# Optimization experiments

Hardware: AMD Instinct MI355X
Metric: run time of the kernel (lower is better)

## Reference

```python
import jax, jax.numpy as jnp
import numpy as np

D_MODEL = 1024
N_HEAD = 16
D_HEAD = D_MODEL // N_HEAD
EXP = 4
B, T = 2, 2048
EPS = 1e-5

def setup_inputs() -> dict:
    key = jax.random.key(0)
    ks = jax.random.split(key, 16)
    s = 0.02
    return {
        "x": jax.random.normal(ks[0], (B, T, D_MODEL), jnp.float32),
        "ln1_w": jnp.ones((D_MODEL,), jnp.float32),
        "ln1_b": jnp.zeros((D_MODEL,), jnp.float32),
        "attn_w": jax.random.normal(ks[1], (D_MODEL, 3 * D_MODEL), jnp.float32) * s,
        "attn_b": jnp.zeros((3 * D_MODEL,), jnp.float32),
        "proj_w": jax.random.normal(ks[2], (D_MODEL, D_MODEL), jnp.float32) * s,
        "proj_b": jnp.zeros((D_MODEL,), jnp.float32),
        "ln2_w": jnp.ones((D_MODEL,), jnp.float32),
        "ln2_b": jnp.zeros((D_MODEL,), jnp.float32),
        "fc_w": jax.random.normal(ks[3], (D_MODEL, EXP * D_MODEL), jnp.float32) * s,
        "fc_b": jnp.zeros((EXP * D_MODEL,), jnp.float32),
        "fc2_w": jax.random.normal(ks[4], (EXP * D_MODEL, D_MODEL), jnp.float32) * s,
        "fc2_b": jnp.zeros((D_MODEL,), jnp.float32),
    }

def _layernorm(x, w, b):
    mu = jnp.mean(x, axis=-1, keepdims=True)
    var = jnp.mean(jnp.square(x - mu), axis=-1, keepdims=True)
    return (x - mu) * jax.lax.rsqrt(var + EPS) * w + b

def _attn(x, attn_w, attn_b, proj_w, proj_b):
    Bx, Tx, C = x.shape
    qkv = x @ attn_w + attn_b  # [B,T,3C]
    q, k, v = jnp.split(qkv, 3, axis=-1)
    # [B, H, T, Dh]
    q = q.reshape(Bx, Tx, N_HEAD, D_HEAD).transpose(0, 2, 1, 3)
    k = k.reshape(Bx, Tx, N_HEAD, D_HEAD).transpose(0, 2, 1, 3)
    v = v.reshape(Bx, Tx, N_HEAD, D_HEAD).transpose(0, 2, 1, 3)
    att = jnp.einsum('bhqd,bhkd->bhqk', q, k) * (1.0 / np.sqrt(D_HEAD))
    causal = jnp.tril(jnp.ones((Tx, Tx), bool))
    att = jnp.where(causal, att, -jnp.inf)
    att = jax.nn.softmax(att, axis=-1)
    y = jnp.einsum('bhqk,bhkd->bhqd', att, v)
    y = y.transpose(0, 2, 1, 3).reshape(Bx, Tx, C)
    return y @ proj_w + proj_b

def reference(x, ln1_w, ln1_b, attn_w, attn_b, proj_w, proj_b,
              ln2_w, ln2_b, fc_w, fc_b, fc2_w, fc2_b):
    x = x + _attn(_layernorm(x, ln1_w, ln1_b), attn_w, attn_b, proj_w, proj_b)
    h = _layernorm(x, ln2_w, ln2_b)
    h = jax.nn.gelu(h @ fc_w + fc_b, approximate=False)  # exact GELU (torch nn.GELU default)
    x = x + (h @ fc2_w + fc2_b)
    return x
```

## Files before the change

### kernel.cpp

```cpp
#include <hip/hip_runtime.h>
#include <hip/hip_bf16.h>
#include <math.h>


#define D_MODEL 1024
#define N_HEAD  16
#define D_HEAD  64
#define SEQ_T   2048
#define BATCH   2
#define NROWS   (BATCH * SEQ_T)
#define C3      (3 * D_MODEL)
#define D_FF    (4 * D_MODEL)

typedef __bf16 bf16x8 __attribute__((ext_vector_type(8)));
typedef __bf16 bf16x4t __attribute__((ext_vector_type(4)));
typedef short  s16x4  __attribute__((ext_vector_type(4)));
typedef float  f32x4  __attribute__((ext_vector_type(4)));

#define WAIT_VM0() asm volatile("s_waitcnt vmcnt(0)" ::: "memory")

__device__ __forceinline__ f32x4 mfma16_bf16(s16x4 a, s16x4 b, f32x4 c)
{
#if __has_builtin(__builtin_amdgcn_mfma_f32_16x16x16_bf16)
    return __builtin_amdgcn_mfma_f32_16x16x16_bf16(
        __builtin_bit_cast(bf16x4t, a), __builtin_bit_cast(bf16x4t, b), c, 0, 0, 0);
#else
    return __builtin_amdgcn_mfma_f32_16x16x16bf16_1k(a, b, c, 0, 0, 0);
#endif
}

__global__ __launch_bounds__(256) void ln_kernel(
    const float* __restrict__ in, const float* __restrict__ w,
    const float* __restrict__ b, __hip_bfloat16* __restrict__ out, int D)
{
    const int row = blockIdx.x;
    const int tid = threadIdx.x;
    const float* x = in + (size_t)row * 1024;

    const float4 v = *(const float4*)(x + tid * 4);
    float s  = v.x + v.y + v.z + v.w;
    float s2 = v.x * v.x + v.y * v.y + v.z * v.z + v.w * v.w;

    __shared__ float rs[256], rs2[256];
    rs[tid] = s; rs2[tid] = s2;
    __syncthreads();
    for (int off = 128; off > 0; off >>= 1) {
        if (tid < off) { rs[tid] += rs[tid + off]; rs2[tid] += rs2[tid + off]; }
        __syncthreads();
    }
    const float mu   = rs[0] * (1.0f / 1024.0f);
    const float var  = rs2[0] * (1.0f / 1024.0f) - mu * mu;
    const float rstd = rsqrtf(var + 1e-5f);

    const float4 w4 = *(const float4*)(w + tid * 4);
    const float4 b4 = *(const float4*)(b + tid * 4);
    float o[4] = {(v.x - mu) * rstd * w4.x + b4.x,
                  (v.y - mu) * rstd * w4.y + b4.y,
                  (v.z - mu) * rstd * w4.z + b4.z,
                  (v.w - mu) * rstd * w4.w + b4.w};
    ushort4 pk;
    { __hip_bfloat16 e0 = __float2bfloat16(o[0]); pk.x = *(unsigned short*)&e0;
      __hip_bfloat16 e1 = __float2bfloat16(o[1]); pk.y = *(unsigned short*)&e1;
      __hip_bfloat16 e2 = __float2bfloat16(o[2]); pk.z = *(unsigned short*)&e2;
      __hip_bfloat16 e3 = __float2bfloat16(o[3]); pk.w = *(unsigned short*)&e3; }
    *(ushort4*)(out + (size_t)row * 1024 + tid * 4) = pk;
}

__global__ __launch_bounds__(256) void transpose_all_kernel(
    const float* __restrict__ attn_w, const float* __restrict__ proj_w,
    const float* __restrict__ fc_w,   const float* __restrict__ fc2_w,
    __hip_bfloat16* __restrict__ attn_wt, __hip_bfloat16* __restrict__ proj_wt,
    __hip_bfloat16* __restrict__ fc_wt,   __hip_bfloat16* __restrict__ fc2_wt)
{
    __shared__ float t[32][33];
    int tb = blockIdx.x;
    const float* W; __hip_bfloat16* Wt; int K, N;
    if (tb < 3072)      { W = attn_w; Wt = attn_wt; K = D_MODEL; N = C3; }
    else if (tb < 4096) { tb -= 3072; W = proj_w; Wt = proj_wt; K = D_MODEL; N = D_MODEL; }
    else if (tb < 8192) { tb -= 4096; W = fc_w;   Wt = fc_wt;   K = D_MODEL; N = D_FF; }
    else                { tb -= 8192; W = fc2_w;  Wt = fc2_wt;  K = D_FF;    N = D_MODEL; }
    const int ntx = N >> 5;
    const int k0 = (tb / ntx) * 32;
    const int n0 = (tb % ntx) * 32;

    const int row = threadIdx.x >> 3;
    const int c4  = (threadIdx.x & 7) * 4;

    const float4 v = *(const float4*)&W[(size_t)(k0 + row) * N + n0 + c4];
    t[row][c4 + 0] = v.x; t[row][c4 + 1] = v.y;
    t[row][c4 + 2] = v.z; t[row][c4 + 3] = v.w;
    __syncthreads();

    ushort4 pk;
    { __hip_bfloat16 e0 = __float2bfloat16(t[c4 + 0][row]); pk.x = *(unsigned short*)&e0;
      __hip_bfloat16 e1 = __float2bfloat16(t[c4 + 1][row]); pk.y = *(unsigned short*)&e1;
      __hip_bfloat16 e2 = __float2bfloat16(t[c4 + 2][row]); pk.z = *(unsigned short*)&e2;
      __hip_bfloat16 e3 = __float2bfloat16(t[c4 + 3][row]); pk.w = *(unsigned short*)&e3; }
    *(ushort4*)&Wt[(size_t)(n0 + row) * K + k0 + c4] = pk;
}

__device__ __forceinline__ void async16(const __hip_bfloat16* g, __hip_bfloat16* l)
{
    __builtin_amdgcn_global_load_lds(
        (const __attribute__((address_space(1))) void*)g,
        (__attribute__((address_space(3))) void*)l, 16, 0, 0);
}

__device__ __forceinline__ float gelu_exact(float v)
{
    return 0.5f * v * (1.0f + erff(v * 0.70710678118654752f));
}

__device__ __forceinline__ void swz_xcd(int& bx, int& by)
{
    const int nbx = gridDim.x;
    const int nwg = nbx * gridDim.y;
    int lin = blockIdx.y * nbx + blockIdx.x;
    const int per = nwg >> 3;
    lin = (lin & 7) * per + (lin >> 3);
    bx = lin % nbx;
    by = lin / nbx;
}


__device__ __forceinline__ void stage_db4(
    const __hip_bfloat16* __restrict__ Ab, const __hip_bfloat16* __restrict__ Bb,
    int K, int kt, __hip_bfloat16* __restrict__ as,
    __hip_bfloat16* __restrict__ bs, int tid)
{
    const int k0 = kt * 32;
#pragma unroll
    for (int i = 0; i < 2; ++i) {
        async16(Ab + (size_t)(i * 64) * K + k0, as + i * 64 * 32 + tid * 8);
        async16(Bb + (size_t)(i * 64) * K + k0, bs + i * 64 * 32 + tid * 8);
    }
}

__device__ __forceinline__ void gemm_db4(
    const __hip_bfloat16* __restrict__ A,
    const __hip_bfloat16* __restrict__ Bt,
    int K, int row0, int col0, f32x4 (&acc)[4][4])
{
    __shared__ __align__(16) __hip_bfloat16 Asl[2][128 * 32];
    __shared__ __align__(16) __hip_bfloat16 Bsl[2][128 * 32];

    const int tid  = threadIdx.x;
    const int wv   = tid >> 6;
    const int lane = tid & 63;
    const int ln15 = lane & 15;
    const int lq   = lane >> 4;
    const int mbase = (wv >> 1) * 64;
    const int nbase = (wv & 1) * 64;
    const int rcol = (lq ^ ((ln15 >> 1) & 3)) * 8;
    const int ssw  = ((tid & 3) ^ ((tid >> 3) & 3)) * 8;
    const __hip_bfloat16* Ab = A  + (size_t)(row0 + (tid >> 2)) * K + ssw;
    const __hip_bfloat16* Bb = Bt + (size_t)(col0 + (tid >> 2)) * K + ssw;
    const int nt = K >> 5;

#pragma unroll
    for (int mi = 0; mi < 4; ++mi)
#pragma unroll
        for (int ni = 0; ni < 4; ++ni) acc[mi][ni] = (f32x4){0.f, 0.f, 0.f, 0.f};

    stage_db4(Ab, Bb, K, 0, &Asl[0][0], &Bsl[0][0], tid);
    WAIT_VM0();
    __builtin_amdgcn_s_barrier();

    for (int t = 0; t < nt; ++t) {
        const int p   = t & 1;
        const int tcl = (t + 1 < nt) ? t + 1 : nt - 1;
        bf16x8 af[4], bfr[4];

#pragma unroll
        for (int mi = 0; mi < 4; ++mi)
            af[mi] = *(const bf16x8*)&Asl[p][(mbase + mi * 16 + ln15) * 32 + rcol];
#pragma unroll
        for (int ni = 0; ni < 4; ++ni)
            bfr[ni] = *(const bf16x8*)&Bsl[p][(nbase + ni * 16 + ln15) * 32 + rcol];

        stage_db4(Ab, Bb, K, tcl, &Asl[p ^ 1][0], &Bsl[p ^ 1][0], tid);

        __builtin_amdgcn_s_setprio(1);
#pragma unroll
        for (int mi = 0; mi < 4; ++mi)
#pragma unroll
            for (int ni = 0; ni < 4; ++ni)
                acc[mi][ni] = __builtin_amdgcn_mfma_f32_16x16x32_bf16(
                    af[mi], bfr[ni], acc[mi][ni], 0, 0, 0);
        __builtin_amdgcn_s_setprio(0);

        WAIT_VM0();
        __builtin_amdgcn_s_barrier();
    }
}


__device__ __forceinline__ void stage_db2w(
    const __hip_bfloat16* __restrict__ Ab, const __hip_bfloat16* __restrict__ Bb,
    int K, int kt, __hip_bfloat16* __restrict__ as,
    __hip_bfloat16* __restrict__ bs, int tid)
{
    const int k0 = kt * 64;
#pragma unroll
    for (int s = 0; s < 2; ++s) {
        async16(Ab + k0 + s * 32, as + s * 64 * 32 + tid * 8);
#pragma unroll
        for (int i = 0; i < 2; ++i)
            async16(Bb + (size_t)(i * 64) * K + k0 + s * 32,
                    bs + s * 128 * 32 + i * 64 * 32 + tid * 8);
    }
}

__device__ __forceinline__ void gemm_db2w(
    const __hip_bfloat16* __restrict__ A,
    const __hip_bfloat16* __restrict__ Bt,
    int K, int row0, int col0, f32x4 (&acc)[2][4])
{
    __shared__ __align__(16) __hip_bfloat16 Asl[2][2 * 64 * 32];
    __shared__ __align__(16) __hip_bfloat16 Bsl[2][2 * 128 * 32];

    const int tid  = threadIdx.x;
    const int wv   = tid >> 6;
    const int lane = tid & 63;
    const int ln15 = lane & 15;
    const int lq   = lane >> 4;
    const int mbase = (wv >> 1) * 32;
    const int nbase = (wv & 1) * 64;
    const int rcol = (lq ^ ((ln15 >> 1) & 3)) * 8;
    const int ssw  = ((tid & 3) ^ ((tid >> 3) & 3)) * 8;
    const __hip_bfloat16* Ab = A  + (size_t)(row0 + (tid >> 2)) * K + ssw;
    const __hip_bfloat16* Bb = Bt + (size_t)(col0 + (tid >> 2)) * K + ssw;
    const int nt = K >> 6;

#pragma unroll
    for (int mi = 0; mi < 2; ++mi)
#pragma unroll
        for (int ni = 0; ni < 4; ++ni) acc[mi][ni] = (f32x4){0.f, 0.f, 0.f, 0.f};

    stage_db2w(Ab, Bb, K, 0, &Asl[0][0], &Bsl[0][0], tid);
    WAIT_VM0();
    __builtin_amdgcn_s_barrier();

    for (int t = 0; t < nt; ++t) {
        const int p   = t & 1;
        const int tcl = (t + 1 < nt) ? t + 1 : nt - 1;
        bf16x8 af[2][2], bfr[2][4];

#pragma unroll
        for (int s = 0; s < 2; ++s) {
#pragma unroll
            for (int mi = 0; mi < 2; ++mi)
                af[s][mi] = *(const bf16x8*)
                    &Asl[p][s * 64 * 32 + (mbase + mi * 16 + ln15) * 32 + rcol];
#pragma unroll
            for (int ni = 0; ni < 4; ++ni)
                bfr[s][ni] = *(const bf16x8*)
                    &Bsl[p][s * 128 * 32 + (nbase + ni * 16 + ln15) * 32 + rcol];
        }

        stage_db2w(Ab, Bb, K, tcl, &Asl[p ^ 1][0], &Bsl[p ^ 1][0], tid);

        __builtin_amdgcn_s_setprio(1);
#pragma unroll
        for (int s = 0; s < 2; ++s)
#pragma unroll
            for (int mi = 0; mi < 2; ++mi)
#pragma unroll
                for (int ni = 0; ni < 4; ++ni)
                    acc[mi][ni] = __builtin_amdgcn_mfma_f32_16x16x32_bf16(
                        af[s][mi], bfr[s][ni], acc[mi][ni], 0, 0, 0);
        __builtin_amdgcn_s_setprio(0);

        WAIT_VM0();
        __builtin_amdgcn_s_barrier();
    }
}

__global__ __launch_bounds__(256, 3) void gemm128_kernel(
    const __hip_bfloat16* __restrict__ A,
    const __hip_bfloat16* __restrict__ Bt,
    const float* __restrict__ bias,
    const float* __restrict__ residual,
    void* __restrict__ Cout,
    int M, int N, int K, int act, int outBf16)
{
    int bx, by;
    swz_xcd(bx, by);
    const int row0 = by * 128;
    const int col0 = bx * 128;

    f32x4 acc[4][4];
    gemm_db4(A, Bt, K, row0, col0, acc);

    const int tid  = threadIdx.x;
    const int wv   = tid >> 6;
    const int lane = tid & 63;
    const int ln15 = lane & 15;
    const int lq   = lane >> 4;
    const int mbase = (wv >> 1) * 64;
    const int nbase = (wv & 1) * 64;

#pragma unroll
    for (int mi = 0; mi < 4; ++mi) {
#pragma unroll
        for (int ni = 0; ni < 4; ++ni) {
            const int gc = col0 + nbase + ni * 16 + ln15;
            const float bv = bias[gc];
#pragma unroll
            for (int r = 0; r < 4; ++r) {
                const int gr = row0 + mbase + mi * 16 + lq * 4 + r;
                float v = acc[mi][ni][r] + bv;
                if (act == 1) v = gelu_exact(v);
                if (residual) v += residual[(size_t)gr * N + gc];
                if (outBf16)
                    ((__hip_bfloat16*)Cout)[(size_t)gr * N + gc] = __float2bfloat16(v);
                else
                    ((float*)Cout)[(size_t)gr * N + gc] = v;
            }
        }
    }
}

__global__ __launch_bounds__(256, 3) void gemm64_kernel(
    const __hip_bfloat16* __restrict__ A,
    const __hip_bfloat16* __restrict__ Bt,
    const float* __restrict__ bias,
    const float* __restrict__ residual,
    void* __restrict__ Cout,
    int M, int N, int K, int act, int outBf16)
{
    int bx, by;
    swz_xcd(bx, by);
    const int row0 = by * 64;
    const int col0 = bx * 128;

    f32x4 acc[2][4];
    gemm_db2w(A, Bt, K, row0, col0, acc);

    const int tid  = threadIdx.x;
    const int wv   = tid >> 6;
    const int lane = tid & 63;
    const int ln15 = lane & 15;
    const int lq   = lane >> 4;
    const int mbase = (wv >> 1) * 32;
    const int nbase = (wv & 1) * 64;

#pragma unroll
    for (int mi = 0; mi < 2; ++mi) {
#pragma unroll
        for (int ni = 0; ni < 4; ++ni) {
            const int gc = col0 + nbase + ni * 16 + ln15;
            const float bv = bias[gc];
#pragma unroll
            for (int r = 0; r < 4; ++r) {
                const int gr = row0 + mbase + mi * 16 + lq * 4 + r;
                float v = acc[mi][ni][r] + bv;
                if (act == 1) v = gelu_exact(v);
                if (residual) v += residual[(size_t)gr * N + gc];
                if (outBf16)
                    ((__hip_bfloat16*)Cout)[(size_t)gr * N + gc] = __float2bfloat16(v);
                else
                    ((float*)Cout)[(size_t)gr * N + gc] = v;
            }
        }
    }
}

__global__ __launch_bounds__(256, 3) void qkv128_kernel(
    const __hip_bfloat16* __restrict__ A,
    const __hip_bfloat16* __restrict__ Bt,
    const float* __restrict__ bias,
    __hip_bfloat16* __restrict__ Qb,
    __hip_bfloat16* __restrict__ Kb,
    __hip_bfloat16* __restrict__ Vtb)
{
    int bx, by;
    swz_xcd(bx, by);
    const int row0 = by * 128;
    const int col0 = bx * 128;

    f32x4 acc[4][4];
    gemm_db4(A, Bt, D_MODEL, row0, col0, acc);

    const int tid  = threadIdx.x;
    const int wv   = tid >> 6;
    const int lane = tid & 63;
    const int ln15 = lane & 15;
    const int lq   = lane >> 4;
    const int mbase = (wv >> 1) * 64;
    const int nbase = (wv & 1) * 64;

#pragma unroll
    for (int mi = 0; mi < 4; ++mi) {
        const int gr0 = row0 + mbase + mi * 16 + lq * 4;
        const int bb  = gr0 >> 11;
        const int q0  = gr0 & 2047;
#pragma unroll
        for (int ni = 0; ni < 4; ++ni) {
            const int gc  = col0 + nbase + ni * 16 + ln15;
            const float bv = bias[gc];
            const int sec = gc >> 10;
            const int hd  = (gc & 1023) >> 6;
            const int d   = gc & 63;
            if (sec == 2) {
                unsigned short u[4];
#pragma unroll
                for (int r = 0; r < 4; ++r) {
                    __hip_bfloat16 e = __float2bfloat16(acc[mi][ni][r] + bv);
                    u[r] = *(unsigned short*)&e;
                }
                uint2 pk;
                pk.x = (unsigned int)u[0] | ((unsigned int)u[1] << 16);
                pk.y = (unsigned int)u[2] | ((unsigned int)u[3] << 16);
                *(uint2*)(Vtb + ((size_t)((bb * N_HEAD + hd) * D_HEAD + d)) * SEQ_T + q0) = pk;
            } else {
                __hip_bfloat16* dst = (sec == 0 ? Qb : Kb)
                    + ((size_t)((bb * N_HEAD + hd) * SEQ_T + q0)) * D_HEAD + d;
#pragma unroll
                for (int r = 0; r < 4; ++r)
                    dst[(size_t)r * D_HEAD] = __float2bfloat16(acc[mi][ni][r] + bv);
            }
        }
    }
}

#define ATQ 64
#define ATK 128
#define NQT (SEQ_T / ATQ)
#define VP2 136

__global__ __launch_bounds__(256) void mfma_attn_kernel(
    const __hip_bfloat16* __restrict__ Qb,
    const __hip_bfloat16* __restrict__ Kb,
    const __hip_bfloat16* __restrict__ Vtb,
    __hip_bfloat16* __restrict__ y)
{
    __shared__ __align__(16) __hip_bfloat16 Ks[2 * ATK * 32];
    __shared__ __align__(16) __hip_bfloat16 Vts[D_HEAD * VP2];

    const int flat = (blockIdx.z * gridDim.y + blockIdx.y) * gridDim.x + blockIdx.x;
    const int xcd  = flat & 7;
    const int slot = flat >> 3;
    const int pair = slot & 15;
    const int hb   = slot >> 4;
    const int h    = xcd + 8 * (hb & 1);
    const int b    = hb >> 1;

    const int tid  = threadIdx.x;
    const int wv   = tid >> 6;
    const int lane = tid & 63;
    const int ln15 = lane & 15;
    const int lq   = lane >> 4;

    const __hip_bfloat16* Qh = Qb  + (size_t)(b * N_HEAD + h) * SEQ_T * D_HEAD;
    const __hip_bfloat16* Kh = Kb  + (size_t)(b * N_HEAD + h) * SEQ_T * D_HEAD;
    const __hip_bfloat16* Vh = Vtb + (size_t)(b * N_HEAD + h) * D_HEAD * SEQ_T;
    const size_t bT = (size_t)b * SEQ_T;

    const float CEXP = 0.18033688011f;

    bf16x8 kreg[4], vreg[4];
    const int kr = tid >> 3, kg = tid & 7;
    const int vr = tid >> 4, vc = tid & 15;
    const int khalf = kg >> 2;
    const int kpos  = (kg & 3) ^ ((kr >> 1) & 3);

    auto issue = [&](int kb) {
#pragma unroll
        for (int i = 0; i < 4; ++i)
            kreg[i] = *(const bf16x8*)(Kh + (size_t)(kb + kr + i * 32) * D_HEAD + kg * 8);
#pragma unroll
        for (int i = 0; i < 4; ++i)
            vreg[i] = *(const bf16x8*)(Vh + (size_t)(vr + i * 16) * SEQ_T + kb + vc * 8);
    };
    auto commit = [&]() {
#pragma unroll
        for (int i = 0; i < 4; ++i) {
            const int r = kr + i * 32;
            *(bf16x8*)&Ks[khalf * (ATK * 32) + r * 32 + kpos * 8] = kreg[i];
        }
#pragma unroll
        for (int i = 0; i < 4; ++i) {
            const int r = vr + i * 16;
            *(bf16x8*)&Vts[r * VP2 + vc * 8] = vreg[i];
        }
    };

    const int rcol = (lq ^ ((ln15 >> 1) & 3)) * 8;

#pragma unroll 1
    for (int half = 0; half < 2; ++half) {
        const int qt    = half == 0 ? pair : (NQT - 1 - pair);
        const int qbase = qt * ATQ;
        const int ntk   = (qt >> 1) + 1;
        const int qg    = qbase + wv * 16 + ln15;

        bf16x8 qf[2];
#pragma unroll
        for (int kc = 0; kc < 2; ++kc)
            qf[kc] = *(const bf16x8*)(Qh + (size_t)(qbase + wv * 16 + ln15) * D_HEAD
                                      + kc * 32 + lq * 8);

        f32x4 Oacc[4];
#pragma unroll
        for (int dn = 0; dn < 4; ++dn) Oacc[dn] = (f32x4){0.f, 0.f, 0.f, 0.f};
        float m_run = -INFINITY, l_run = 0.f;

        issue(0);

        for (int t = 0; t < ntk; ++t) {
            const int kb = t * ATK;
            commit();
            __syncthreads();
            if (t + 1 < ntk) issue((t + 1) * ATK);

            f32x4 st[8];
#pragma unroll
            for (int jf = 0; jf < 8; ++jf) st[jf] = (f32x4){0.f, 0.f, 0.f, 0.f};
            __builtin_amdgcn_s_setprio(1);
#pragma unroll
            for (int jf = 0; jf < 8; ++jf) {
                const int rw = jf * 16 + ln15;
                const bf16x8 kf0 = *(const bf16x8*)&Ks[rw * 32 + rcol];
                const bf16x8 kf1 = *(const bf16x8*)&Ks[ATK * 32 + rw * 32 + rcol];
                st[jf] = __builtin_amdgcn_mfma_f32_16x16x32_bf16(kf0, qf[0], st[jf], 0, 0, 0);
                st[jf] = __builtin_amdgcn_mfma_f32_16x16x32_bf16(kf1, qf[1], st[jf], 0, 0, 0);
            }
            __builtin_amdgcn_s_setprio(0);

            if (t == ntk - 1) {
#pragma unroll
                for (int jf = 0; jf < 8; ++jf)
#pragma unroll
                    for (int r = 0; r < 4; ++r)
                        if ((kb + jf * 16 + lq * 4 + r) > qg) st[jf][r] = -INFINITY;
            }

            float tmax = st[0][0];
#pragma unroll
            for (int jf = 0; jf < 8; ++jf)
#pragma unroll
                for (int r = 0; r < 4; ++r) tmax = fmaxf(tmax, st[jf][r]);
            tmax = fmaxf(tmax, __shfl_xor(tmax, 16));
            tmax = fmaxf(tmax, __shfl_xor(tmax, 32));
            const float mnew  = fmaxf(m_run, tmax);
            const float alpha = exp2f((m_run - mnew) * CEXP);
            const float mc    = mnew * CEXP;
            float psum = 0.f;
#pragma unroll
            for (int jf = 0; jf < 8; ++jf)
#pragma unroll
                for (int r = 0; r < 4; ++r) {
                    const float p = exp2f(fmaf(st[jf][r], CEXP, -mc));
                    st[jf][r] = p;
                    psum += p;
                }
            psum += __shfl_xor(psum, 16);
            psum += __shfl_xor(psum, 32);
            l_run = alpha * l_run + psum;
            m_run = mnew;

            float a4[4];
#pragma unroll
            for (int r = 0; r < 4; ++r) a4[r] = __shfl(alpha, lq * 4 + r);
#pragma unroll
            for (int dn = 0; dn < 4; ++dn)
#pragma unroll
                for (int r = 0; r < 4; ++r) Oacc[dn][r] *= a4[r];

            __builtin_amdgcn_s_setprio(1);
#pragma unroll
            for (int jf = 0; jf < 8; ++jf) {
                s16x4 pfr;
#pragma unroll
                for (int s = 0; s < 4; ++s) {
                    __hip_bfloat16 e = __float2bfloat16(st[jf][s]);
                    pfr[s] = __builtin_bit_cast(short, e);
                }
#pragma unroll
                for (int dn = 0; dn < 4; ++dn) {
                    const s16x4 vfr = *(const s16x4*)&Vts[(dn * 16 + ln15) * VP2
                                                          + jf * 16 + lq * 4];
                    Oacc[dn] = mfma16_bf16(pfr, vfr, Oacc[dn]);
                }
            }
            __builtin_amdgcn_s_setprio(0);
            __syncthreads();
        }

        float il[4];
#pragma unroll
        for (int r = 0; r < 4; ++r) il[r] = 1.0f / __shfl(l_run, lq * 4 + r);
#pragma unroll
        for (int dn = 0; dn < 4; ++dn)
#pragma unroll
            for (int r = 0; r < 4; ++r)
                Ks[(wv * 16 + lq * 4 + r) * 72 + dn * 16 + ln15] =
                    __float2bfloat16(Oacc[dn][r] * il[r]);
        const int r2 = lane >> 3, c8 = (lane & 7) * 8;
#pragma unroll
        for (int i = 0; i < 2; ++i) {
            const int row = wv * 16 + r2 + 8 * i;
            const bf16x8 val = *(const bf16x8*)&Ks[row * 72 + c8];
            *(bf16x8*)(y + (bT + qbase + row) * D_MODEL + h * D_HEAD + c8) = val;
        }
        __syncthreads();
    }
}

extern "C" void kernel_launch(void* const* d_in, const int* in_sizes, int n_in,
                              void* d_out, int out_size, void* d_ws, size_t ws_size,
                              hipStream_t stream)
{
    const float* x      = (const float*)d_in[0];
    const float* ln1_w  = (const float*)d_in[1];
    const float* ln1_b  = (const float*)d_in[2];
    const float* attn_w = (const float*)d_in[3];
    const float* attn_b = (const float*)d_in[4];
    const float* proj_w = (const float*)d_in[5];
    const float* proj_b = (const float*)d_in[6];
    const float* ln2_w  = (const float*)d_in[7];
    const float* ln2_b  = (const float*)d_in[8];
    const float* fc_w   = (const float*)d_in[9];
    const float* fc_b   = (const float*)d_in[10];
    const float* fc2_w  = (const float*)d_in[11];
    const float* fc2_b  = (const float*)d_in[12];
    float* out = (float*)d_out;

    char* ws = (char*)d_ws;
    __hip_bfloat16* Qb      = (__hip_bfloat16*)(ws);
    __hip_bfloat16* Kb      = (__hip_bfloat16*)(ws + (size_t)8  * 1024 * 1024);
    __hip_bfloat16* Vtb     = (__hip_bfloat16*)(ws + (size_t)16 * 1024 * 1024);
    __hip_bfloat16* h_bf    = (__hip_bfloat16*)(ws);
    __hip_bfloat16* ln_buf  = (__hip_bfloat16*)(ws + (size_t)32 * 1024 * 1024);
    __hip_bfloat16* y_buf   = (__hip_bfloat16*)(ws + (size_t)40 * 1024 * 1024);
    float*          xmid    = (float*)(ws + (size_t)48 * 1024 * 1024);
    __hip_bfloat16* attn_wt = (__hip_bfloat16*)(ws + (size_t)64 * 1024 * 1024);
    __hip_bfloat16* proj_wt = (__hip_bfloat16*)(ws + (size_t)70 * 1024 * 1024);
    __hip_bfloat16* fc_wt   = (__hip_bfloat16*)(ws + (size_t)72 * 1024 * 1024);
    __hip_bfloat16* fc2_wt  = (__hip_bfloat16*)(ws + (size_t)80 * 1024 * 1024);

    dim3 blk256(256);

    transpose_all_kernel<<<dim3(12288), blk256, 0, stream>>>(
        attn_w, proj_w, fc_w, fc2_w, attn_wt, proj_wt, fc_wt, fc2_wt);

    ln_kernel<<<dim3(NROWS), blk256, 0, stream>>>(x, ln1_w, ln1_b, ln_buf, D_MODEL);

    qkv128_kernel<<<dim3(C3 / 128, NROWS / 128), blk256, 0, stream>>>(
        ln_buf, attn_wt, attn_b, Qb, Kb, Vtb);

    mfma_attn_kernel<<<dim3(NQT / 2, N_HEAD, BATCH), blk256, 0, stream>>>(
        Qb, Kb, Vtb, y_buf);

    gemm64_kernel<<<dim3(D_MODEL / 128, NROWS / 64), blk256, 0, stream>>>(
        y_buf, proj_wt, proj_b, x, xmid, NROWS, D_MODEL, D_MODEL, 0, 0);

    ln_kernel<<<dim3(NROWS), blk256, 0, stream>>>(xmid, ln2_w, ln2_b, ln_buf, D_MODEL);

    gemm128_kernel<<<dim3(D_FF / 128, NROWS / 128), blk256, 0, stream>>>(
        ln_buf, fc_wt, fc_b, nullptr, h_bf, NROWS, D_FF, D_MODEL, 1, 1);

    gemm64_kernel<<<dim3(D_MODEL / 128, NROWS / 64), blk256, 0, stream>>>(
        h_bf, fc2_wt, fc2_b, xmid, out, NROWS, D_MODEL, D_FF, 0, 0);
}
```

Baseline: 356.9 us.

## Add 256x256 8-wave pipelined GEMM for FC layer with tanh-GELU

Measured after the change: 341.6 us. -4.3%, faster.

```diff
diff --git a/kernel.cpp b/kernel.cpp
--- a/kernel.cpp
+++ b/kernel.cpp
@@ -18,6 +18,8 @@
 typedef float  f32x4  __attribute__((ext_vector_type(4)));
 
 #define WAIT_VM0() asm volatile("s_waitcnt vmcnt(0)" ::: "memory")
+#define WAIT_VM2() asm volatile("s_waitcnt vmcnt(2)" ::: "memory")
+#define WAIT_VM4() asm volatile("s_waitcnt vmcnt(4)" ::: "memory")
 
 __device__ __forceinline__ f32x4 mfma16_bf16(s16x4 a, s16x4 b, f32x4 c)
 {
@@ -106,9 +108,10 @@
         (__attribute__((address_space(3))) void*)l, 16, 0, 0);
 }
 
-__device__ __forceinline__ float gelu_exact(float v)
-{
-    return 0.5f * v * (1.0f + erff(v * 0.70710678118654752f));
+__device__ __forceinline__ float gelu_fast(float v)
+{
+    const float t = v * (0.7978845608f + 0.0356774081f * v * v);
+    return v / (1.0f + exp2f(-2.885390082f * t));
 }
 
 __device__ __forceinline__ void swz_xcd(int& bx, int& by)
@@ -122,6 +125,159 @@
     by = lin / nbx;
 }
 
+
+__global__ __launch_bounds__(512, 1) void gemm8p_kernel(
+    const __hip_bfloat16* __restrict__ A,
+    const __hip_bfloat16* __restrict__ Bt,
+    const float* __restrict__ bias,
+    __hip_bfloat16* __restrict__ Cout,
+    int M, int N, int K, int act)
+{
+    __shared__ __align__(16) __hip_bfloat16 Asl[2][4][64 * 64];
+    __shared__ __align__(16) __hip_bfloat16 Bsl[2][2][128 * 64];
+
+    int bx, by;
+    swz_xcd(bx, by);
+    const int row0 = by * 256;
+    const int col0 = bx * 256;
+
+    const int tid  = threadIdx.x;
+    const int wv   = tid >> 6;
+    const int lane = tid & 63;
+    const int ln15 = lane & 15;
+    const int lq   = lane >> 4;
+    const int wr   = wv >> 2;
+    const int wc   = wv & 3;
+
+    const int srow = tid >> 3;
+    const int sg   = ((tid & 7) ^ ((tid >> 3) & 7)) * 8;
+    const __hip_bfloat16* Ab = A  + (size_t)(row0 + srow) * K + sg;
+    const __hip_bfloat16* Bb = Bt + (size_t)(col0 + srow) * K + sg;
+    const int nt = K >> 6;
+
+    f32x4 acc[8][4];
+#pragma unroll
+    for (int mi = 0; mi < 8; ++mi)
+#pragma unroll
+        for (int ni = 0; ni < 4; ++ni) acc[mi][ni] = (f32x4){0.f, 0.f, 0.f, 0.f};
+
+    auto stA = [&](int t, int buf, int b) {
+        async16(Ab + (size_t)(b * 64) * K + t * 64, &Asl[buf][b][0] + tid * 8);
+    };
+    auto stB = [&](int t, int buf, int h) {
+        async16(Bb + (size_t)(h * 128) * K + t * 64, &Bsl[buf][h][0] + tid * 8);
+        async16(Bb + (size_t)(h * 128 + 64) * K + t * 64,
+                &Bsl[buf][h][0] + 4096 + tid * 8);
+    };
+
+    const int rg0 = (lq ^ (ln15 & 7)) * 8;
+    const int rg1 = ((4 | lq) ^ (ln15 & 7)) * 8;
+    auto ldA = [&](int buf, int mi, int kk) -> bf16x8 {
+        return *(const bf16x8*)&Asl[buf][wr * 2 + (mi >> 2)]
+            [((mi & 3) * 16 + ln15) * 64 + (kk ? rg1 : rg0)];
+    };
+    auto ldB = [&](int buf, int ni, int kk) -> bf16x8 {
+        return *(const bf16x8*)&Bsl[buf][wc >> 1]
+            [((wc & 1) * 64 + ni * 16 + ln15) * 64 + (kk ? rg1 : rg0)];
+    };
+
+    stB(0, 0, 0); stB(0, 0, 1);
+    stA(0, 0, 0); stA(0, 0, 2); stA(0, 0, 1); stA(0, 0, 3);
+    WAIT_VM0();
+    __builtin_amdgcn_s_barrier();
+
+    for (int t = 0; t < nt; ++t) {
+        const int pp = t & 1, op = pp ^ 1;
+        const int tc = (t + 1 < nt) ? t + 1 : nt - 1;
+        bf16x8 af[2][2], bfr[4][2];
+
+#pragma unroll
+        for (int m = 0; m < 2; ++m) { af[m][0] = ldA(pp, m, 0); af[m][1] = ldA(pp, m, 1); }
+#pragma unroll
+        for (int ni = 0; ni < 4; ++ni) { bfr[ni][0] = ldB(pp, ni, 0); bfr[ni][1] = ldB(pp, ni, 1); }
+        stB(tc, op, 0);
+        __builtin_amdgcn_s_barrier();
+        __builtin_amdgcn_s_setprio(1);
+#pragma unroll
+        for (int kk = 0; kk < 2; ++kk)
+#pragma unroll
+            for (int m = 0; m < 2; ++m)
+#pragma unroll
+                for (int ni = 0; ni < 4; ++ni)
+                    acc[m][ni] = __builtin_amdgcn_mfma_f32_16x16x32_bf16(
+                        af[m][kk], bfr[ni][kk], acc[m][ni], 0, 0, 0);
+        __builtin_amdgcn_s_setprio(0);
+        __builtin_amdgcn_s_barrier();
+
+#pragma unroll
+        for (int m = 0; m < 2; ++m) { af[m][0] = ldA(pp, 2 + m, 0); af[m][1] = ldA(pp, 2 + m, 1); }
+        stB(tc, op, 1);
+        WAIT_VM4();
+        __builtin_amdgcn_s_barrier();
+        __builtin_amdgcn_s_setprio(1);
+#pragma unroll
+        for (int kk = 0; kk < 2; ++kk)
+#pragma unroll
+            for (int m = 0; m < 2; ++m)
+#pragma unroll
+                for (int ni = 0; ni < 4; ++ni)
+                    acc[2 + m][ni] = __builtin_amdgcn_mfma_f32_16x16x32_bf16(
+                        af[m][kk], bfr[ni][kk], acc[2 + m][ni], 0, 0, 0);
+        __builtin_amdgcn_s_setprio(0);
+        __builtin_amdgcn_s_barrier();
+
+#pragma unroll
+        for (int m = 0; m < 2; ++m) { af[m][0] = ldA(pp, 4 + m, 0); af[m][1] = ldA(pp, 4 + m, 1); }
+        stA(tc, op, 0); stA(tc, op, 2);
+        __builtin_amdgcn_s_barrier();
+        __builtin_amdgcn_s_setprio(1);
+#pragma unroll
+        for (int kk = 0; kk < 2; ++kk)
+#pragma unroll
+            for (int m = 0; m < 2; ++m)
+#pragma unroll
+                for (int ni = 0; ni < 4; ++ni)
+                    acc[4 + m][ni] = __builtin_amdgcn_mfma_f32_16x16x32_bf16(
+                        af[m][kk], bfr[ni][kk], acc[4 + m][ni], 0, 0, 0);
+        __builtin_amdgcn_s_setprio(0);
+        __builtin_amdgcn_s_barrier();
+
+#pragma unroll
+        for (int m = 0; m < 2; ++m) { af[m][0] = ldA(pp, 6 + m, 0); af[m][1] = ldA(pp, 6 + m, 1); }
+        stA(tc, op, 1); stA(tc, op, 3);
+        WAIT_VM2();
+        __builtin_amdgcn_s_barrier();
+        __builtin_amdgcn_s_setprio(1);
+#pragma unroll
+        for (int kk = 0; kk < 2; ++kk)
+#pragma unroll
+            for (int m = 0; m < 2; ++m)
+#pragma unroll
+                for (int ni = 0; ni < 4; ++ni)
+                    acc[6 + m][ni] = __builtin_amdgcn_mfma_f32_16x16x32_bf16(
+                        af[m][kk], bfr[ni][kk], acc[6 + m][ni], 0, 0, 0);
+        __builtin_amdgcn_s_setprio(0);
+        __builtin_amdgcn_s_barrier();
+    }
+
+    const int mbase = wr * 128;
+    const int nbase = wc * 64;
+#pragma unroll
+    for (int mi = 0; mi < 8; ++mi) {
+#pragma unroll
+        for (int ni = 0; ni < 4; ++ni) {
+            const int gc = col0 + nbase + ni * 16 + ln15;
+            const float bv = bias[gc];
+#pragma unroll
+            for (int r = 0; r < 4; ++r) {
+                const int gr = row0 + mbase + mi * 16 + lq * 4 + r;
+                float v = acc[mi][ni][r] + bv;
+                if (act == 1) v = gelu_fast(v);
+                Cout[(size_t)gr * N + gc] = __float2bfloat16(v);
+            }
+        }
+    }
+}
 
 __device__ __forceinline__ void stage_db4(
     const __hip_bfloat16* __restrict__ Ab, const __hip_bfloat16* __restrict__ Bb,
@@ -194,7 +350,6 @@
     }
 }
 
-
 __device__ __forceinline__ void stage_db2w(
     const __hip_bfloat16* __restrict__ Ab, const __hip_bfloat16* __restrict__ Bb,
     int K, int kt, __hip_bfloat16* __restrict__ as,
@@ -276,51 +431,6 @@
     }
 }
 
-__global__ __launch_bounds__(256, 3) void gemm128_kernel(
-    const __hip_bfloat16* __restrict__ A,
-    const __hip_bfloat16* __restrict__ Bt,
-    const float* __restrict__ bias,
-    const float* __restrict__ residual,
-    void* __restrict__ Cout,
-    int M, int N, int K, int act, int outBf16)
-{
-    int bx, by;
-    swz_xcd(bx, by);
-    const int row0 = by * 128;
-    const int col0 = bx * 128;
-
-    f32x4 acc[4][4];
-    gemm_db4(A, Bt, K, row0, col0, acc);
-
-    const int tid  = threadIdx.x;
-    const int wv   = tid >> 6;
-    const int lane = tid & 63;
-    const int ln15 = lane & 15;
-    const int lq   = lane >> 4;
-    const int mbase = (wv >> 1) * 64;
-    const int nbase = (wv & 1) * 64;
-
-#pragma unroll
-    for (int mi = 0; mi < 4; ++mi) {
-#pragma unroll
-        for (int ni = 0; ni < 4; ++ni) {
-            const int gc = col0 + nbase + ni * 16 + ln15;
-            const float bv = bias[gc];
-#pragma unroll
-            for (int r = 0; r < 4; ++r) {
-                const int gr = row0 + mbase + mi * 16 + lq * 4 + r;
-                float v = acc[mi][ni][r] + bv;
-                if (act == 1) v = gelu_exact(v);
-                if (residual) v += residual[(size_t)gr * N + gc];
-                if (outBf16)
-                    ((__hip_bfloat16*)Cout)[(size_t)gr * N + gc] = __float2bfloat16(v);
-                else
-                    ((float*)Cout)[(size_t)gr * N + gc] = v;
-            }
-        }
-    }
-}
-
 __global__ __launch_bounds__(256, 3) void gemm64_kernel(
     const __hip_bfloat16* __restrict__ A,
     const __hip_bfloat16* __restrict__ Bt,
@@ -355,7 +465,7 @@
             for (int r = 0; r < 4; ++r) {
                 const int gr = row0 + mbase + mi * 16 + lq * 4 + r;
                 float v = acc[mi][ni][r] + bv;
-                if (act == 1) v = gelu_exact(v);
+                if (act == 1) v = gelu_fast(v);
                 if (residual) v += residual[(size_t)gr * N + gc];
                 if (outBf16)
                     ((__hip_bfloat16*)Cout)[(size_t)gr * N + gc] = __float2bfloat16(v);
@@ -641,6 +751,7 @@
     __hip_bfloat16* fc2_wt  = (__hip_bfloat16*)(ws + (size_t)80 * 1024 * 1024);
 
     dim3 blk256(256);
+    dim3 blk512(512);
 
     transpose_all_kernel<<<dim3(12288), blk256, 0, stream>>>(
         attn_w, proj_w, fc_w, fc2_w, attn_wt, proj_wt, fc_wt, fc2_wt);
@@ -658,8 +769,8 @@
 
     ln_kernel<<<dim3(NROWS), blk256, 0, stream>>>(xmid, ln2_w, ln2_b, ln_buf, D_MODEL);
 
-    gemm128_kernel<<<dim3(D_FF / 128, NROWS / 128), blk256, 0, stream>>>(
-        ln_buf, fc_wt, fc_b, nullptr, h_bf, NROWS, D_FF, D_MODEL, 1, 1);
+    gemm8p_kernel<<<dim3(D_FF / 256, NROWS / 256), blk512, 0, stream>>>(
+        ln_buf, fc_wt, fc_b, h_bf, NROWS, D_FF, D_MODEL, 1);
 
     gemm64_kernel<<<dim3(D_MODEL / 128, NROWS / 64), blk256, 0, stream>>>(
         h_bf, fc2_wt, fc2_b, xmid, out, NROWS, D_MODEL, D_FF, 0, 0);
```
